# Performance work log

Measured on AMD Instinct MI355X. Metric: run time of the kernel, lower is better.

Reference implementation:

```python
import jax, jax.numpy as jnp
import numpy as np

W_BIT = 4
OUT_F = 11008
IN_F = 4096
K = 16


def unpack_sign(q_bytes):
    """q_bytes: [n_bytes] int32 holding uint8 values. Little-endian bit order.
    Returns float32 signs in {-1, +1} of shape [OUT_F, IN_F]."""
    bits = (q_bytes[:, None] >> jnp.arange(8, dtype=q_bytes.dtype)) & 1  # [n_bytes, 8]
    signs = (2 * bits - 1).astype(jnp.float32)
    return signs.reshape(OUT_F, IN_F)


def setup_inputs() -> dict:
    key = jax.random.key(0)
    k0, k1, k2, k3 = jax.random.split(key, 4)
    x = jax.random.normal(k0, (4, 2048, IN_F), dtype=jnp.float32)
    # packed sign bits: one byte stores 8 signs; OUT_F*IN_F//8 bytes per bit-plane
    qweight = jax.random.randint(k1, (W_BIT, OUT_F * IN_F // 8), 0, 256, dtype=jnp.int32)
    u = jax.random.normal(k2, (W_BIT, OUT_F, K), dtype=jnp.float32) * 0.05
    vt = jax.random.normal(k3, (W_BIT, K, IN_F), dtype=jnp.float32) * 0.05
    return {"x": x, "qweight": qweight, "u": u, "vt": vt}


def reference(x, qweight, u, vt):
    # Reconstruct full weight: w = sum_i sign_i * (u_i @ vt_i), then GEMM x @ w.T.
    # Loop over the small fixed w_bit count to avoid holding all [OUT,IN] bit-planes at once.
    w = jnp.zeros((OUT_F, IN_F), dtype=x.dtype)
    for i in range(W_BIT):
        signs = unpack_sign(qweight[i])            # [OUT_F, IN_F]
        w = w + signs * (u[i] @ vt[i])             # rank-K reconstruction masked by signs
    return x @ w.T                                  # [B, S, OUT_F]
```

## Files before the change

kernel.cpp:

```cpp
#include <hip/hip_runtime.h>
#include <hip/hip_bf16.h>

#define W_BIT 4
#define OUT_F 11008
#define IN_F 4096
#define KRANK 16
#define M_DIM 8192
#define QW_PLANE (OUT_F * IN_F / 8)

#define N_DIM OUT_F
#define K_DIM 4096
#define NT 64
#define NBN 43

typedef __attribute__((ext_vector_type(8))) short short8;
typedef __attribute__((ext_vector_type(4))) float f32x4;

__device__ __forceinline__ short f2bf(float f) {
    union { float f; unsigned u; } v;
    v.f = f;
    unsigned r = v.u + 0x7fffu + ((v.u >> 16) & 1u);
    return (short)(r >> 16);
}

__device__ __forceinline__ void async16(void* lds_p, const void* g) {
    __builtin_amdgcn_global_load_lds(
        (const __attribute__((address_space(1))) unsigned int*)g,
        (__attribute__((address_space(3))) unsigned int*)lds_p,
        16, 0, 0);
}

#define BAR() __builtin_amdgcn_s_barrier()
#define LGKM0() do { asm volatile("s_waitcnt lgkmcnt(0)" ::: "memory"); \
                     __builtin_amdgcn_sched_barrier(0); } while (0)
#define VMC(n) do { asm volatile("s_waitcnt vmcnt(" #n ")" ::: "memory"); \
                    __builtin_amdgcn_sched_barrier(0); } while (0)
#define PRIO1() __builtin_amdgcn_s_setprio(1)
#define PRIO0() __builtin_amdgcn_s_setprio(0)

__global__ __launch_bounds__(256) void convert_x_kernel(
    const float* __restrict__ x, short* __restrict__ xb) {
    int tid = blockIdx.x * blockDim.x + threadIdx.x;
    int stride = gridDim.x * blockDim.x;
    const int n8 = (M_DIM * IN_F) / 8;
    for (int i = tid; i < n8; i += stride) {
        f32x4 a = ((const f32x4*)x)[2 * i];
        f32x4 b = ((const f32x4*)x)[2 * i + 1];
        short8 o;
        o[0] = f2bf(a[0]); o[1] = f2bf(a[1]); o[2] = f2bf(a[2]); o[3] = f2bf(a[3]);
        o[4] = f2bf(b[0]); o[5] = f2bf(b[1]); o[6] = f2bf(b[2]); o[7] = f2bf(b[3]);
        ((short8*)xb)[i] = o;
    }
}

__global__ __launch_bounds__(256) void reconstruct_w_kernel(
    const int* __restrict__ qw, const float* __restrict__ u,
    const float* __restrict__ vt, short* __restrict__ wb) {
    __shared__ float vts[W_BIT][KRANK][128];
    __shared__ float us[W_BIT][KRANK][64];

    const int t = threadIdx.x;
    const int o0 = blockIdx.y * 64;
    const int c0 = blockIdx.x * 128;

    for (int idx = t; idx < W_BIT * KRANK * 128; idx += 256) {
        int i = idx >> 11, rem = idx & 2047, k = rem >> 7, c = rem & 127;
        vts[i][k][c] = vt[(i * KRANK + k) * IN_F + c0 + c];
    }
    for (int idx = t; idx < W_BIT * KRANK * 64; idx += 256) {
        int i = idx >> 10, rem = idx & 1023, o = rem >> 4, k = rem & 15;
        us[i][k][o] = u[((size_t)i * OUT_F + o0 + o) * KRANK + k];
    }
    __syncthreads();

    const int to = (t >> 4) * 4;
    const int tc = (t & 15) * 8;

    float wacc[4][8];
#pragma unroll
    for (int r = 0; r < 4; ++r)
#pragma unroll
        for (int c = 0; c < 8; ++c) wacc[r][c] = 0.f;

#pragma unroll
    for (int i = 0; i < W_BIT; ++i) {
        float dot[4][8];
#pragma unroll
        for (int r = 0; r < 4; ++r)
#pragma unroll
            for (int c = 0; c < 8; ++c) dot[r][c] = 0.f;
#pragma unroll
        for (int k = 0; k < KRANK; ++k) {
            f32x4 uv = *(const f32x4*)&us[i][k][to];
            f32x4 v0 = *(const f32x4*)&vts[i][k][tc];
            f32x4 v1 = *(const f32x4*)&vts[i][k][tc + 4];
#pragma unroll
            for (int r = 0; r < 4; ++r) {
#pragma unroll
                for (int c = 0; c < 4; ++c) {
                    dot[r][c]     += uv[r] * v0[c];
                    dot[r][c + 4] += uv[r] * v1[c];
                }
            }
        }
#pragma unroll
        for (int r = 0; r < 4; ++r) {
            unsigned byte = (unsigned)qw[i * QW_PLANE + (((o0 + to + r) * IN_F + c0 + tc) >> 3)];
#pragma unroll
            for (int c = 0; c < 8; ++c)
                wacc[r][c] += ((byte >> c) & 1u) ? dot[r][c] : -dot[r][c];
        }
    }
#pragma unroll
    for (int r = 0; r < 4; ++r) {
        short8 o8;
#pragma unroll
        for (int c = 0; c < 8; ++c) o8[c] = f2bf(wacc[r][c]);
        *(short8*)&wb[(size_t)(o0 + to + r) * IN_F + c0 + tc] = o8;
    }
}

__global__ __launch_bounds__(512, 2) void gemm256_kernel(
    const short* __restrict__ A, const short* __restrict__ B, float* __restrict__ C) {
    extern __shared__ short lds[];

    const int t = threadIdx.x;
    const int lane = t & 63, wid = t >> 6;
    const int wr = wid >> 2, wc = wid & 3;
    const int fr = lane & 15, fq = lane >> 4;

    const int bid = blockIdx.x;
    const int cpx = gridDim.x >> 3;
    const int swzb = (bid & 7) * cpx + (bid >> 3);
    const int bm = swzb / NBN, bn = swzb % NBN;
    const long row0 = (long)bm * 256, col0 = (long)bn * 256;

    const int colswz = (fq ^ ((fr >> 1) & 3)) * 8;
    const int aoff = (wr * 128 + fr) * 32 + colswz;
    const int boff = 32768 + (wc * 64 + fr) * 32 + colswz;

    const int srow = t >> 2;
    const int sswz = (((t & 3) ^ ((srow >> 1) & 3)) << 3);
    const short* pA0 = A + (row0 + srow) * (size_t)K_DIM + sswz;
    const short* pA1 = pA0 + (size_t)128 * K_DIM;
    const short* pB0 = B + (col0 + srow) * (size_t)K_DIM + sswz;
    const short* pB1 = pB0 + (size_t)128 * K_DIM;
    const int ldst0 = t * 8;

    f32x4 acc[8][4];
#pragma unroll
    for (int m = 0; m < 8; ++m)
#pragma unroll
        for (int n = 0; n < 4; ++n) acc[m][n] = (f32x4)0.f;

    short8 af[4], bf0[4], bf1[4];

#define STG(P0, P1, SLOT, OFFB) do {                                   \
    async16(&lds[(SLOT) + ldst0], (const char*)(P0) + (OFFB));         \
    async16(&lds[(SLOT) + 4096 + ldst0], (const char*)(P1) + (OFFB));  \
} while (0)

#define RDA(KSLOT, MH) do {                                            \
    _Pragma("unroll") for (int m = 0; m < 4; ++m)                      \
        af[m] = *(const short8*)&lds[(KSLOT) + ((MH) * 4 + m) * 512 + aoff]; \
} while (0)

#define RDB(DST, KSLOT) do {                                           \
    _Pragma("unroll") for (int n = 0; n < 4; ++n)                      \
        DST[n] = *(const short8*)&lds[(KSLOT) + n * 512 + boff];       \
} while (0)

#define MFQ(BF, MH) do {                                               \
    _Pragma("unroll") for (int m = 0; m < 4; ++m)                      \
        _Pragma("unroll") for (int n = 0; n < 4; ++n)                  \
            acc[(MH) * 4 + m][n] = __builtin_amdgcn_mfma_f32_16x16x32_bf16( \
                af[m], BF[n], acc[(MH) * 4 + m][n], 0, 0, 0);          \
} while (0)

#define MMA(BF, MH) do { PRIO1(); MFQ(BF, MH); PRIO0();                \
    __builtin_amdgcn_sched_barrier(0); } while (0)

    STG(pA0, pA1, 0,     0);
    STG(pB0, pB1, 32768, 0);
    STG(pA0, pA1, 8192,  64);
    STG(pB0, pB1, 40960, 64);
    STG(pA0, pA1, 16384, 128);
    STG(pB0, pB1, 49152, 128);
    VMC(4);
    BAR();

    for (int it = 0; it < 31; ++it) {
        RDB(bf0, 0); RDA(0, 0);
        STG(pA0, pA1, 24576, 192);
        BAR(); LGKM0(); MMA(bf0, 0);
        RDA(0, 1);
        STG(pB0, pB1, 57344, 192);
        BAR(); LGKM0(); MMA(bf0, 1);
        RDB(bf1, 8192); RDA(8192, 0);
        STG(pA0, pA1, 0, 256);
        BAR(); LGKM0(); MMA(bf1, 0);
        RDA(8192, 1);
        STG(pB0, pB1, 32768, 256);
        VMC(4);
        BAR(); LGKM0(); MMA(bf1, 1);

        RDB(bf0, 16384); RDA(16384, 0);
        STG(pA0, pA1, 8192, 320);
        BAR(); LGKM0(); MMA(bf0, 0);
        RDA(16384, 1);
        STG(pB0, pB1, 40960, 320);
        BAR(); LGKM0(); MMA(bf0, 1);
        RDB(bf1, 24576); RDA(24576, 0);
        STG(pA0, pA1, 16384, 384);
        BAR(); LGKM0(); MMA(bf1, 0);
        RDA(24576, 1);
        STG(pB0, pB1, 49152, 384);
        VMC(4);
        BAR(); LGKM0(); MMA(bf1, 1);

        pA0 += 128; pA1 += 128; pB0 += 128; pB1 += 128;
    }

    RDB(bf0, 0); RDA(0, 0);
    STG(pA0, pA1, 24576, 192);
    BAR(); LGKM0(); MMA(bf0, 0);
    RDA(0, 1);
    STG(pB0, pB1, 57344, 192);
    BAR(); LGKM0(); MMA(bf0, 1);
    RDB(bf1, 8192); RDA(8192, 0);
    BAR(); LGKM0(); MMA(bf1, 0);
    RDA(8192, 1);
    VMC(0);
    BAR(); LGKM0(); MMA(bf1, 1);
    RDB(bf0, 16384); RDA(16384, 0);
    BAR(); LGKM0(); MMA(bf0, 0);
    RDA(16384, 1);
    BAR(); LGKM0(); MMA(bf0, 1);
    RDB(bf1, 24576); RDA(24576, 0);
    BAR(); LGKM0(); MMA(bf1, 0);
    RDA(24576, 1);
    BAR(); LGKM0(); MMA(bf1, 1);

#pragma unroll
    for (int m = 0; m < 8; ++m) {
#pragma unroll
        for (int n = 0; n < 4; ++n) {
            f32x4 v = acc[m][n];
            long r0 = row0 + wr * 128 + m * 16 + fq * 4;
            long cc = col0 + wc * 64 + n * 16 + fr;
#pragma unroll
            for (int jj = 0; jj < 4; ++jj)
                C[(size_t)(r0 + jj) * N_DIM + cc] = v[jj];
        }
    }
#undef STG
#undef RDA
#undef RDB
#undef MFQ
#undef MMA
}

extern "C" void kernel_launch(void* const* d_in, const int* in_sizes, int n_in,
                              void* d_out, int out_size, void* d_ws, size_t ws_size,
                              hipStream_t stream) {
    const float* x  = (const float*)d_in[0];
    const int*   qw = (const int*)d_in[1];
    const float* u  = (const float*)d_in[2];
    const float* vt = (const float*)d_in[3];
    float* out = (float*)d_out;

    const size_t wb_bytes = (size_t)OUT_F * IN_F * 2;
    short* wb = (short*)d_ws;
    short* xb = (short*)((char*)d_ws + wb_bytes);

    (void)hipFuncSetAttribute((const void*)gemm256_kernel,
                              hipFuncAttributeMaxDynamicSharedMemorySize, 131072);

    hipLaunchKernelGGL(convert_x_kernel, dim3(2048), dim3(256), 0, stream, x, xb);
    hipLaunchKernelGGL(reconstruct_w_kernel, dim3(IN_F / 128, OUT_F / 64), dim3(256), 0, stream,
                       qw, u, vt, wb);
    hipLaunchKernelGGL(gemm256_kernel, dim3((M_DIM / 256) * (N_DIM / 256)), dim3(512), 131072,
                       stream, xb, wb, out);
}
```

Before: 881.7 us.

## Software-pipeline LDS fragment reads with double-buffered A registers and partial lgkm waits

The bf16 GEMM main loop now issues the LDS reads for the next half-step before the current MFMA block. It keeps two A-fragment register sets (afA/afB), and waits with lgkmcnt(4) or lgkmcnt(8) instead of draining to zero. LDS reads become inline-asm ds_read_b128 with compile-time immediate offsets from precomputed base addresses, which cuts per-read address arithmetic. The aim is to hide LDS latency behind MFMA work, at the cost of more VGPRs and fragile hand-counted waitcnt ordering.

```diff
diff --git a/kernel.cpp b/kernel.cpp
--- a/kernel.cpp
+++ b/kernel.cpp
@@ -31,12 +31,15 @@
 }
 
 #define BAR() __builtin_amdgcn_s_barrier()
-#define LGKM0() do { asm volatile("s_waitcnt lgkmcnt(0)" ::: "memory"); \
+#define LGKM(n) do { asm volatile("s_waitcnt lgkmcnt(" #n ")" ::: "memory"); \
                      __builtin_amdgcn_sched_barrier(0); } while (0)
 #define VMC(n) do { asm volatile("s_waitcnt vmcnt(" #n ")" ::: "memory"); \
                     __builtin_amdgcn_sched_barrier(0); } while (0)
 #define PRIO1() __builtin_amdgcn_s_setprio(1)
 #define PRIO0() __builtin_amdgcn_s_setprio(0)
+
+#define DSR(DST, AV, IMM) \
+    asm volatile("ds_read_b128 %0, %1 offset:%2" : "=v"(DST) : "v"(AV), "n"(IMM))
 
 __global__ __launch_bounds__(256) void convert_x_kernel(
     const float* __restrict__ x, short* __restrict__ xb) {
@@ -139,6 +142,9 @@
     const int aoff = (wr * 128 + fr) * 32 + colswz;
     const int boff = 32768 + (wc * 64 + fr) * 32 + colswz;
 
+    const unsigned av = (unsigned)(size_t)((__attribute__((address_space(3))) short*)lds + aoff);
+    const unsigned bv = (unsigned)(size_t)((__attribute__((address_space(3))) short*)lds + boff);
+
     const int srow = t >> 2;
     const int sswz = (((t & 3) ^ ((srow >> 1) & 3)) << 3);
     const short* pA0 = A + (row0 + srow) * (size_t)K_DIM + sswz;
@@ -153,32 +159,33 @@
 #pragma unroll
         for (int n = 0; n < 4; ++n) acc[m][n] = (f32x4)0.f;
 
-    short8 af[4], bf0[4], bf1[4];
+    short8 afA[4], afB[4], bf0[4], bf1[4];
 
 #define STG(P0, P1, SLOT, OFFB) do {                                   \
     async16(&lds[(SLOT) + ldst0], (const char*)(P0) + (OFFB));         \
     async16(&lds[(SLOT) + 4096 + ldst0], (const char*)(P1) + (OFFB));  \
 } while (0)
 
-#define RDA(KSLOT, MH) do {                                            \
-    _Pragma("unroll") for (int m = 0; m < 4; ++m)                      \
-        af[m] = *(const short8*)&lds[(KSLOT) + ((MH) * 4 + m) * 512 + aoff]; \
+#define RDA(SET, KSLOT, MH) do {                                       \
+    DSR(SET[0], av, ((KSLOT) + ((MH) * 4 + 0) * 512) * 2);             \
+    DSR(SET[1], av, ((KSLOT) + ((MH) * 4 + 1) * 512) * 2);             \
+    DSR(SET[2], av, ((KSLOT) + ((MH) * 4 + 2) * 512) * 2);             \
+    DSR(SET[3], av, ((KSLOT) + ((MH) * 4 + 3) * 512) * 2);             \
 } while (0)
 
 #define RDB(DST, KSLOT) do {                                           \
-    _Pragma("unroll") for (int n = 0; n < 4; ++n)                      \
-        DST[n] = *(const short8*)&lds[(KSLOT) + n * 512 + boff];       \
+    DSR(DST[0], bv, ((KSLOT) - 32768 + 0 * 512) * 2);                  \
+    DSR(DST[1], bv, ((KSLOT) - 32768 + 1 * 512) * 2);                  \
+    DSR(DST[2], bv, ((KSLOT) - 32768 + 2 * 512) * 2);                  \
+    DSR(DST[3], bv, ((KSLOT) - 32768 + 3 * 512) * 2);                  \
 } while (0)
 
-#define MFQ(BF, MH) do {                                               \
+#define MMA(AF, BF, MH) do { PRIO1();                                  \
     _Pragma("unroll") for (int m = 0; m < 4; ++m)                      \
         _Pragma("unroll") for (int n = 0; n < 4; ++n)                  \
             acc[(MH) * 4 + m][n] = __builtin_amdgcn_mfma_f32_16x16x32_bf16( \
-                af[m], BF[n], acc[(MH) * 4 + m][n], 0, 0, 0);          \
-} while (0)
-
-#define MMA(BF, MH) do { PRIO1(); MFQ(BF, MH); PRIO0();                \
-    __builtin_amdgcn_sched_barrier(0); } while (0)
+                AF[m], BF[n], acc[(MH) * 4 + m][n], 0, 0, 0);          \
+    PRIO0(); __builtin_amdgcn_sched_barrier(0); } while (0)
 
     STG(pA0, pA1, 0,     0);
     STG(pB0, pB1, 32768, 0);
@@ -188,58 +195,58 @@
     STG(pB0, pB1, 49152, 128);
     VMC(4);
     BAR();
+    RDA(afA, 0, 0); RDB(bf0, 32768);
 
     for (int it = 0; it < 31; ++it) {
-        RDB(bf0, 0); RDA(0, 0);
+        RDA(afB, 0, 1);
         STG(pA0, pA1, 24576, 192);
-        BAR(); LGKM0(); MMA(bf0, 0);
-        RDA(0, 1);
+        BAR(); LGKM(4); MMA(afA, bf0, 0);
+        RDB(bf1, 40960); RDA(afA, 8192, 0);
         STG(pB0, pB1, 57344, 192);
-        BAR(); LGKM0(); MMA(bf0, 1);
-        RDB(bf1, 8192); RDA(8192, 0);
+        BAR(); LGKM(8); MMA(afB, bf0, 1);
+        RDA(afB, 8192, 1);
         STG(pA0, pA1, 0, 256);
-        BAR(); LGKM0(); MMA(bf1, 0);
-        RDA(8192, 1);
+        BAR(); LGKM(4); MMA(afA, bf1, 0);
         STG(pB0, pB1, 32768, 256);
         VMC(4);
-        BAR(); LGKM0(); MMA(bf1, 1);
-
-        RDB(bf0, 16384); RDA(16384, 0);
+        RDB(bf0, 49152); RDA(afA, 16384, 0);
+        BAR(); LGKM(8); MMA(afB, bf1, 1);
+
+        RDA(afB, 16384, 1);
         STG(pA0, pA1, 8192, 320);
-        BAR(); LGKM0(); MMA(bf0, 0);
-        RDA(16384, 1);
+        BAR(); LGKM(4); MMA(afA, bf0, 0);
+        RDB(bf1, 57344); RDA(afA, 24576, 0);
         STG(pB0, pB1, 40960, 320);
-        BAR(); LGKM0(); MMA(bf0, 1);
-        RDB(bf1, 24576); RDA(24576, 0);
+        BAR(); LGKM(8); MMA(afB, bf0, 1);
+        RDA(afB, 24576, 1);
         STG(pA0, pA1, 16384, 384);
-        BAR(); LGKM0(); MMA(bf1, 0);
-        RDA(24576, 1);
+        BAR(); LGKM(4); MMA(afA, bf1, 0);
         STG(pB0, pB1, 49152, 384);
         VMC(4);
-        BAR(); LGKM0(); MMA(bf1, 1);
+        RDB(bf0, 32768); RDA(afA, 0, 0);
+        BAR(); LGKM(8); MMA(afB, bf1, 1);
 
         pA0 += 128; pA1 += 128; pB0 += 128; pB1 += 128;
     }
 
-    RDB(bf0, 0); RDA(0, 0);
+    RDA(afB, 0, 1);
     STG(pA0, pA1, 24576, 192);
-    BAR(); LGKM0(); MMA(bf0, 0);
-    RDA(0, 1);
+    BAR(); LGKM(4); MMA(afA, bf0, 0);
+    RDB(bf1, 40960); RDA(afA, 8192, 0);
     STG(pB0, pB1, 57344, 192);
-    BAR(); LGKM0(); MMA(bf0, 1);
-    RDB(bf1, 8192); RDA(8192, 0);
-    BAR(); LGKM0(); MMA(bf1, 0);
-    RDA(8192, 1);
+    BAR(); LGKM(8); MMA(afB, bf0, 1);
+    RDA(afB, 8192, 1);
+    BAR(); LGKM(4); MMA(afA, bf1, 0);
     VMC(0);
-    BAR(); LGKM0(); MMA(bf1, 1);
-    RDB(bf0, 16384); RDA(16384, 0);
-    BAR(); LGKM0(); MMA(bf0, 0);
-    RDA(16384, 1);
-    BAR(); LGKM0(); MMA(bf0, 1);
-    RDB(bf1, 24576); RDA(24576, 0);
-    BAR(); LGKM0(); MMA(bf1, 0);
-    RDA(24576, 1);
-    BAR(); LGKM0(); MMA(bf1, 1);
+    RDB(bf0, 49152); RDA(afA, 16384, 0);
+    BAR(); LGKM(8); MMA(afB, bf1, 1);
+    RDA(afB, 16384, 1);
+    BAR(); LGKM(4); MMA(afA, bf0, 0);
+    RDB(bf1, 57344); RDA(afA, 24576, 0);
+    BAR(); LGKM(8); MMA(afB, bf0, 1);
+    RDA(afB, 24576, 1);
+    BAR(); LGKM(4); MMA(afA, bf1, 0);
+    BAR(); LGKM(0); MMA(afB, bf1, 1);
 
 #pragma unroll
     for (int m = 0; m < 8; ++m) {
@@ -256,7 +263,6 @@
 #undef STG
 #undef RDA
 #undef RDB
-#undef MFQ
 #undef MMA
 }
 
```

After: 875.5 us. About the same (-0.7%).
